# Performance work log

Hardware: AMD Instinct MI355X
Metric: run time of the kernel (lower is better)

The kernel has to match this reference:

```python
import jax, jax.numpy as jnp
import numpy as np

B, N, QD, H, D = 2, 2048, 1152, 16, 72
INNER = H * D
RETAIN_RATE = 0.4  # layer_count in [4, 64] branch
N_KEEP = int(N * RETAIN_RATE)
N_PRUNE = N - N_KEEP
SCALE = D ** (-0.5)


def setup_inputs() -> dict:
    key = jax.random.key(0)
    ks = jax.random.split(key, 6)
    s = 0.02
    return {
        "x": jax.random.normal(ks[0], (B, N, QD), jnp.float32),
        "Wq": jax.random.normal(ks[1], (QD, INNER), jnp.float32) * s,
        "Wk": jax.random.normal(ks[2], (QD, INNER), jnp.float32) * s,
        "Wv": jax.random.normal(ks[3], (QD, INNER), jnp.float32) * s,
        "Wo": jax.random.normal(ks[4], (INNER, QD), jnp.float32) * s,
        "bo": jnp.zeros((QD,), jnp.float32),
    }


def reference(x, Wq, Wk, Wv, Wo, bo):
    b = x.shape[0]
    # self-attention: context = x
    q = (x @ Wq).reshape(b, N, H, D).transpose(0, 2, 1, 3)  # [b,H,N,D]
    k = (x @ Wk).reshape(b, N, H, D).transpose(0, 2, 1, 3)
    v = (x @ Wv).reshape(b, N, H, D).transpose(0, 2, 1, 3)

    # ---- WPR pruning pass: full attention map, mean over heads ----
    logits = jnp.einsum('bhnd,bhmd->bhnm', q, k) * SCALE  # [b,H,N,N]
    M = jax.nn.softmax(logits, axis=-1)
    attn = M.mean(axis=1)  # [b,N,N]

    # 5-step power iteration: dist = (1/N) @ attn^5
    dist = jnp.full((b, 1, N), 1.0 / N, dtype=attn.dtype)
    for _ in range(5):
        dist = dist @ attn
    importance = dist[:, 0]  # [b,N]

    _, imp_inds = jax.lax.top_k(importance, N_KEEP)
    _, prune_inds = jax.lax.top_k(-importance, N_PRUNE)
    # boolean-mask selection in torch returns rows in ascending index order
    sorted_imp = jnp.sort(imp_inds, axis=1)      # [b,N_KEEP]
    sorted_prune = jnp.sort(prune_inds, axis=1)  # [b,N_PRUNE]

    selected_rows = jnp.take_along_axis(attn, sorted_imp[:, :, None], axis=1)  # [b,N_KEEP,N]
    max_inds = jnp.argmax(selected_rows, axis=1)  # [b,N]: most-attending retained row per token
    sim_inds = jnp.take_along_axis(max_inds, sorted_prune, axis=1)  # [b,N_PRUNE]

    # ---- attention among retained tokens only ----
    gi = sorted_imp[:, None, :, None]  # broadcast gather index
    q_r = jnp.take_along_axis(q, gi, axis=2)  # [b,H,N_KEEP,D]
    k_r = jnp.take_along_axis(k, gi, axis=2)
    v_r = jnp.take_along_axis(v, gi, axis=2)
    attn_r = jax.nn.softmax(jnp.einsum('bhnd,bhmd->bhnm', q_r, k_r) * SCALE, axis=-1)
    out_r = jnp.einsum('bhnm,bhmd->bhnd', attn_r, v_r)  # [b,H,N_KEEP,D]
    out_r = out_r.transpose(0, 2, 1, 3).reshape(b, N_KEEP, INNER)

    # similarity-based recovery for pruned tokens
    out_p = jnp.take_along_axis(out_r, sim_inds[:, :, None], axis=1)  # [b,N_PRUNE,INNER]

    bidx = jnp.arange(b)[:, None]
    out = jnp.zeros((b, N, INNER), out_r.dtype)
    out = out.at[bidx, sorted_imp].set(out_r)
    out = out.at[bidx, sorted_prune].set(out_p)

    return out @ Wo + bo
```

## Files before the change

### kernel.cpp

```cpp
#include <hip/hip_runtime.h>

namespace {
constexpr int B = 2;
constexpr int N = 2048;
constexpr int QD = 1152;
constexpr int H = 16;
constexpr int D = 72;
constexpr int INNER = 1152;
constexpr int NKEEP = 819;
constexpr int PSL = 32;
constexpr int ILEN = N / PSL;
constexpr int DP = 80;
constexpr int LSTR = 88;
constexpr int ASL = 8;
constexpr int ACH = (NKEEP + ASL - 1) / ASL;
}

#define FINF __builtin_inff()
#define SCALE 0.11785113019775793f

typedef __attribute__((ext_vector_type(8))) __bf16 bf16x8;
typedef __attribute__((ext_vector_type(16))) float f32x16;
typedef __attribute__((ext_vector_type(8))) short short8;

__device__ __forceinline__ f32x16 mfma_bf16(bf16x8 a, bf16x8 b, f32x16 c) {
  return __builtin_amdgcn_mfma_f32_32x32x16_bf16(a, b, c, 0, 0, 0);
}
__device__ __forceinline__ short f2bf(float x) {
  unsigned u = __float_as_uint(x);
  unsigned r = (u + 0x7fffu + ((u >> 16) & 1u)) >> 16;
  return (short)r;
}
__device__ __forceinline__ float bf2f(short b) {
  return __uint_as_float(((unsigned)(unsigned short)b) << 16);
}

__global__ __launch_bounds__(256) void k_xsplit(
    const float* __restrict__ X, short* __restrict__ Xh, short* __restrict__ Xl,
    int total)
{
  int g = blockIdx.x * 256 + threadIdx.x;
  if (g >= total) return;
  float v = X[g];
  short hb = f2bf(v);
  Xh[g] = hb;
  Xl[g] = f2bf(v - bf2f(hb));
}

__global__ __launch_bounds__(256) void k_wsplitT(
    const float* __restrict__ W, short* __restrict__ WTh, short* __restrict__ WTl)
{
  __shared__ float tile[64][65];
  const int tid = threadIdx.x;
  const int k0 = blockIdx.y * 64, n0 = blockIdx.x * 64;
  {
    int r = tid >> 2, c0 = (tid & 3) * 16;
#pragma unroll
    for (int j = 0; j < 16; j += 4) {
      float4 v = *(const float4*)&W[(size_t)(k0 + r) * 1152 + n0 + c0 + j];
      tile[r][c0 + j] = v.x; tile[r][c0 + j + 1] = v.y;
      tile[r][c0 + j + 2] = v.z; tile[r][c0 + j + 3] = v.w;
    }
  }
  __syncthreads();
  for (int e = tid; e < 4096; e += 256) {
    int nr = e >> 6, kc = e & 63;
    float v = tile[kc][nr];
    short hb = f2bf(v);
    WTh[(size_t)(n0 + nr) * 1152 + k0 + kc] = hb;
    WTl[(size_t)(n0 + nr) * 1152 + k0 + kc] = f2bf(v - bf2f(hb));
  }
}

__global__ __launch_bounds__(256, 2) void k_pgemm3(
    const short* __restrict__ Ah_g, const short* __restrict__ Al_g,
    const short* __restrict__ Bh_g, const short* __restrict__ Bl_g,
    short* __restrict__ QKV0)
{
  constexpr int LK = 40;
  __shared__ short AhS[256 * LK], AlS[256 * LK];
  __shared__ short BhS[128 * LK], BlS[128 * LK];
  const int tid = threadIdx.x;
  const int wv = tid >> 6, ln = tid & 63;
  const int col = ln & 31, hi = ln >> 5;
  const int wm = wv >> 1, wn = wv & 1;
  const int m0 = blockIdx.y * 256, n0 = blockIdx.x * 128;
  f32x16 acc[4][2];
#pragma unroll
  for (int mi = 0; mi < 4; ++mi)
#pragma unroll
    for (int ni = 0; ni < 2; ++ni)
#pragma unroll
      for (int r = 0; r < 16; ++r) acc[mi][ni][r] = 0.f;

  for (int kt = 0; kt < 1152; kt += 32) {
    __syncthreads();
    for (int e = tid; e < 1024; e += 256) {
      int r = e >> 2, c4 = e & 3;
      size_t sa = (size_t)(m0 + r) * 1152 + kt + c4 * 8;
      *(float4*)&AhS[r * LK + c4 * 8] = *(const float4*)(Ah_g + sa);
      *(float4*)&AlS[r * LK + c4 * 8] = *(const float4*)(Al_g + sa);
    }
    for (int e = tid; e < 512; e += 256) {
      int r = e >> 2, c4 = e & 3;
      size_t sb = (size_t)(n0 + r) * 1152 + kt + c4 * 8;
      *(float4*)&BhS[r * LK + c4 * 8] = *(const float4*)(Bh_g + sb);
      *(float4*)&BlS[r * LK + c4 * 8] = *(const float4*)(Bl_g + sb);
    }
    __syncthreads();
#pragma unroll
    for (int kc = 0; kc < 2; ++kc) {
      bf16x8 ah[4], al[4], bh[2], bl[2];
#pragma unroll
      for (int mi = 0; mi < 4; ++mi) {
        int r = wm * 128 + mi * 32 + col;
        ah[mi] = *(const bf16x8*)&AhS[r * LK + kc * 16 + hi * 8];
        al[mi] = *(const bf16x8*)&AlS[r * LK + kc * 16 + hi * 8];
      }
#pragma unroll
      for (int ni = 0; ni < 2; ++ni) {
        int r = wn * 64 + ni * 32 + col;
        bh[ni] = *(const bf16x8*)&BhS[r * LK + kc * 16 + hi * 8];
        bl[ni] = *(const bf16x8*)&BlS[r * LK + kc * 16 + hi * 8];
      }
#pragma unroll
      for (int mi = 0; mi < 4; ++mi)
#pragma unroll
        for (int ni = 0; ni < 2; ++ni) {
          acc[mi][ni] = mfma_bf16(ah[mi], bh[ni], acc[mi][ni]);
          acc[mi][ni] = mfma_bf16(ah[mi], bl[ni], acc[mi][ni]);
          acc[mi][ni] = mfma_bf16(al[mi], bh[ni], acc[mi][ni]);
        }
    }
  }
  const size_t S = (size_t)65536 * 80;
#pragma unroll
  for (int mi = 0; mi < 4; ++mi)
#pragma unroll
    for (int ni = 0; ni < 2; ++ni)
#pragma unroll
      for (int r = 0; r < 16; ++r) {
        int m = m0 + wm * 128 + mi * 32 + (r & 3) + 8 * (r >> 2) + 4 * hi;
        int c = n0 + wn * 64 + ni * 32 + col;
        int which = c / 1152, cm = c - which * 1152;
        int hh = cm / 72, dd = cm - hh * 72;
        int b = m >> 11, nn = m & 2047;
        size_t idx = (((size_t)(b * 16 + hh)) * 2048 + nn) * 80 + dd;
        float v = acc[mi][ni][r];
        short hb = f2bf(v);
        short* OH = QKV0 + (size_t)which * 2 * S;
        OH[idx] = hb;
        OH[S + idx] = f2bf(v - bf2f(hb));
      }
}

__global__ __launch_bounds__(256, 2) void k_stats3(
    const short* __restrict__ Qh, const short* __restrict__ Ql,
    const short* __restrict__ Kh, const short* __restrict__ Kl,
    float* __restrict__ inv_out)
{
  __shared__ __align__(16) short kh[64 * LSTR];
  __shared__ __align__(16) short kl[64 * LSTR];
  const int tid = threadIdx.x;
  const int wv = tid >> 6, ln = tid & 63;
  const int col = ln & 31, hi = ln >> 5;
  const int q0 = blockIdx.x * 256;
  const int h = blockIdx.y, b = blockIdx.z;
  const size_t bhbase = (size_t)(b * H + h) * N * DP;

  bf16x8 qfh[2][5], qfl[2][5];
#pragma unroll
  for (int mi = 0; mi < 2; ++mi) {
    const size_t rb = bhbase + (size_t)(q0 + wv * 64 + mi * 32 + col) * DP + hi * 8;
#pragma unroll
    for (int d = 0; d < 5; ++d) {
      qfh[mi][d] = *(const bf16x8*)(const void*)(Qh + rb + d * 16);
      qfl[mi][d] = *(const bf16x8*)(const void*)(Ql + rb + d * 16);
    }
  }
  float s[2][16];
#pragma unroll
  for (int mi = 0; mi < 2; ++mi)
#pragma unroll
    for (int r = 0; r < 16; ++r) s[mi][r] = 0.f;

  float4 rkh[3], rkl[3];
  auto LOADK = [&](int kt) {
#pragma unroll
    for (int ss = 0; ss < 3; ++ss) {
      int e = ss * 256 + tid;
      if (e < 640) {
        int r = e / 10, cc = e - r * 10;
        size_t sb = bhbase + (size_t)(kt + r) * DP + cc * 8;
        rkh[ss] = *(const float4*)(const void*)(Kh + sb);
        rkl[ss] = *(const float4*)(const void*)(Kl + sb);
      }
    }
  };
  auto STOREK = [&]() {
#pragma unroll
    for (int ss = 0; ss < 3; ++ss) {
      int e = ss * 256 + tid;
      if (e < 640) {
        int r = e / 10, cc = e - r * 10;
        *(float4*)(void*)(kh + r * LSTR + cc * 8) = rkh[ss];
        *(float4*)(void*)(kl + r * LSTR + cc * 8) = rkl[ss];
      }
    }
  };

  LOADK(0);
  for (int kt = 0; kt < N; kt += 64) {
    __syncthreads();
    STOREK();
    __syncthreads();
    if (kt + 64 < N) LOADK(kt + 64);
    f32x16 z[2][2];
#pragma unroll
    for (int mi = 0; mi < 2; ++mi)
#pragma unroll
      for (int rn = 0; rn < 2; ++rn)
#pragma unroll
        for (int r = 0; r < 16; ++r) z[mi][rn][r] = 0.f;
#pragma unroll
    for (int d = 0; d < 5; ++d) {
      const int boff = d * 16 + hi * 8;
      bf16x8 bh0 = *(const bf16x8*)(const void*)(kh + col * LSTR + boff);
      bf16x8 bl0 = *(const bf16x8*)(const void*)(kl + col * LSTR + boff);
      bf16x8 bh1 = *(const bf16x8*)(const void*)(kh + (32 + col) * LSTR + boff);
      bf16x8 bl1 = *(const bf16x8*)(const void*)(kl + (32 + col) * LSTR + boff);
#pragma unroll
      for (int mi = 0; mi < 2; ++mi) {
        z[mi][0] = mfma_bf16(qfh[mi][d], bh0, z[mi][0]);
        z[mi][0] = mfma_bf16(qfh[mi][d], bl0, z[mi][0]);
        z[mi][0] = mfma_bf16(qfl[mi][d], bh0, z[mi][0]);
        z[mi][1] = mfma_bf16(qfh[mi][d], bh1, z[mi][1]);
        z[mi][1] = mfma_bf16(qfh[mi][d], bl1, z[mi][1]);
        z[mi][1] = mfma_bf16(qfl[mi][d], bh1, z[mi][1]);
      }
    }
#pragma unroll
    for (int mi = 0; mi < 2; ++mi)
#pragma unroll
      for (int r = 0; r < 16; ++r)
        s[mi][r] += __expf(z[mi][0][r] * SCALE) + __expf(z[mi][1][r] * SCALE);
  }
#pragma unroll
  for (int mi = 0; mi < 2; ++mi)
#pragma unroll
    for (int r = 0; r < 16; ++r) {
      float v = s[mi][r];
#pragma unroll
      for (int o = 1; o < 32; o <<= 1) v += __shfl_xor(v, o);
      if (col == 0) {
        int row = q0 + wv * 64 + mi * 32 + ((r & 3) + ((r >> 2) << 3) + (hi << 2));
        inv_out[(size_t)(b * H + h) * N + row] = 1.0f / v;
      }
    }
}

__global__ __launch_bounds__(256, 2) void k_attn3(
    const short* __restrict__ Qh, const short* __restrict__ Ql,
    const short* __restrict__ Kh, const short* __restrict__ Kl,
    const float* __restrict__ inv_in, float* __restrict__ attn)
{
  __shared__ __align__(16) short kh[64 * LSTR];
  __shared__ __align__(16) short kl[64 * LSTR];
  __shared__ float invs[256];
  const int tid = threadIdx.x;
  const int wv = tid >> 6, ln = tid & 63;
  const int col = ln & 31, hi = ln >> 5;
  const int k0 = blockIdx.x * 64, q0 = blockIdx.y * 256, b = blockIdx.z;

  f32x16 pa[2][2];
#pragma unroll
  for (int mi = 0; mi < 2; ++mi)
#pragma unroll
    for (int rn = 0; rn < 2; ++rn)
#pragma unroll
      for (int r = 0; r < 16; ++r) pa[mi][rn][r] = 0.f;

  float4 rkh[3], rkl[3];
  float rin;
  auto LOADH = [&](int h) {
    const size_t hb = (size_t)(b * H + h) * N * DP;
#pragma unroll
    for (int ss = 0; ss < 3; ++ss) {
      int e = ss * 256 + tid;
      if (e < 640) {
        int r = e / 10, cc = e - r * 10;
        size_t sb = hb + (size_t)(k0 + r) * DP + cc * 8;
        rkh[ss] = *(const float4*)(const void*)(Kh + sb);
        rkl[ss] = *(const float4*)(const void*)(Kl + sb);
      }
    }
    rin = inv_in[(size_t)(b * H + h) * N + q0 + tid];
  };
  auto STOREH = [&]() {
#pragma unroll
    for (int ss = 0; ss < 3; ++ss) {
      int e = ss * 256 + tid;
      if (e < 640) {
        int r = e / 10, cc = e - r * 10;
        *(float4*)(void*)(kh + r * LSTR + cc * 8) = rkh[ss];
        *(float4*)(void*)(kl + r * LSTR + cc * 8) = rkl[ss];
      }
    }
    invs[tid] = rin;
  };

  LOADH(0);
  for (int h = 0; h < H; ++h) {
    __syncthreads();
    STOREH();
    __syncthreads();
    if (h + 1 < H) LOADH(h + 1);

    const size_t bhbase = (size_t)(b * H + h) * N * DP;
    f32x16 z[2][2];
#pragma unroll
    for (int mi = 0; mi < 2; ++mi)
#pragma unroll
      for (int rn = 0; rn < 2; ++rn)
#pragma unroll
        for (int r = 0; r < 16; ++r) z[mi][rn][r] = 0.f;

#pragma unroll
    for (int d = 0; d < 5; ++d) {
      const int boff = d * 16 + hi * 8;
      bf16x8 bh0 = *(const bf16x8*)(const void*)(kh + col * LSTR + boff);
      bf16x8 bl0 = *(const bf16x8*)(const void*)(kl + col * LSTR + boff);
      bf16x8 bh1 = *(const bf16x8*)(const void*)(kh + (32 + col) * LSTR + boff);
      bf16x8 bl1 = *(const bf16x8*)(const void*)(kl + (32 + col) * LSTR + boff);
      bf16x8 qh0 = *(const bf16x8*)(const void*)(Qh + bhbase + (size_t)(q0 + wv * 64 + col) * DP + boff);
      bf16x8 ql0 = *(const bf16x8*)(const void*)(Ql + bhbase + (size_t)(q0 + wv * 64 + col) * DP + boff);
      bf16x8 qh1 = *(const bf16x8*)(const void*)(Qh + bhbase + (size_t)(q0 + wv * 64 + 32 + col) * DP + boff);
      bf16x8 ql1 = *(const bf16x8*)(const void*)(Ql + bhbase + (size_t)(q0 + wv * 64 + 32 + col) * DP + boff);
      z[0][0] = mfma_bf16(qh0, bh0, z[0][0]);
      z[0][0] = mfma_bf16(qh0, bl0, z[0][0]);
      z[0][0] = mfma_bf16(ql0, bh0, z[0][0]);
      z[0][1] = mfma_bf16(qh0, bh1, z[0][1]);
      z[0][1] = mfma_bf16(qh0, bl1, z[0][1]);
      z[0][1] = mfma_bf16(ql0, bh1, z[0][1]);
      z[1][0] = mfma_bf16(qh1, bh0, z[1][0]);
      z[1][0] = mfma_bf16(qh1, bl0, z[1][0]);
      z[1][0] = mfma_bf16(ql1, bh0, z[1][0]);
      z[1][1] = mfma_bf16(qh1, bh1, z[1][1]);
      z[1][1] = mfma_bf16(qh1, bl1, z[1][1]);
      z[1][1] = mfma_bf16(ql1, bh1, z[1][1]);
    }
#pragma unroll
    for (int mi = 0; mi < 2; ++mi)
#pragma unroll
      for (int r = 0; r < 16; ++r) {
        const int rloc = wv * 64 + mi * 32 + (r & 3) + ((r >> 2) << 3) + (hi << 2);
        const float iv = invs[rloc];
        pa[mi][0][r] += __expf(z[mi][0][r] * SCALE) * iv;
        pa[mi][1][r] += __expf(z[mi][1][r] * SCALE) * iv;
      }
  }
  const float invH = 1.0f / H;
#pragma unroll
  for (int mi = 0; mi < 2; ++mi)
#pragma unroll
    for (int r = 0; r < 16; ++r) {
      const int row = q0 + wv * 64 + mi * 32 + (r & 3) + ((r >> 2) << 3) + (hi << 2);
      attn[((size_t)b * N + row) * N + k0 + col] = pa[mi][0][r] * invH;
      attn[((size_t)b * N + row) * N + k0 + 32 + col] = pa[mi][1][r] * invH;
    }
}

__global__ __launch_bounds__(256) void k_power(
    const float* __restrict__ attn, const float* __restrict__ din,
    float* __restrict__ partial, int first)
{
  int g = blockIdx.x * 256 + threadIdx.x;
  int sy = blockIdx.y;
  int b = g / N, j = g % N;
  const float* ab = attn + (size_t)b * N * N;
  int i0 = sy * ILEN;
  float sum = 0.f;
  if (first) {
    for (int i = i0; i < i0 + ILEN; ++i) sum += ab[(size_t)i * N + j];
    sum *= (1.0f / N);
  } else {
    const float* db = din + b * N;
    for (int i = i0; i < i0 + ILEN; ++i) sum += db[i] * ab[(size_t)i * N + j];
  }
  partial[(size_t)sy * (B * N) + g] = sum;
}

__global__ __launch_bounds__(256) void k_powred(
    const float* __restrict__ partial, float* __restrict__ dout)
{
  int g = blockIdx.x * 256 + threadIdx.x;
  if (g >= B * N) return;
  float s = 0.f;
  for (int sy = 0; sy < PSL; ++sy) s += partial[(size_t)sy * (B * N) + g];
  dout[g] = s;
}

__global__ __launch_bounds__(1024) void k_partition(
    const float* __restrict__ imp, int* __restrict__ sorted_imp,
    int* __restrict__ keepflag, int* __restrict__ s_map)
{
  __shared__ float v[N];
  __shared__ int   id[N];
  __shared__ int   kf[N];
  __shared__ int   ps[N];
  const int tid = threadIdx.x;
  const int b = blockIdx.x;
  for (int i = tid; i < N; i += 1024) { v[i] = imp[b * N + i]; id[i] = i; }
  for (int k = 2; k <= N; k <<= 1) {
    for (int j = k >> 1; j > 0; j >>= 1) {
      __syncthreads();
      for (int i = tid; i < N; i += 1024) {
        int ixj = i ^ j;
        if (ixj > i) {
          bool up = ((i & k) == 0);
          float va = v[i], vb = v[ixj];
          int ia = id[i], ib = id[ixj];
          bool b_before_a = (vb > va) || (vb == va && ib < ia);
          if (b_before_a == up) { v[i] = vb; v[ixj] = va; id[i] = ib; id[ixj] = ia; }
        }
      }
    }
  }
  __syncthreads();
  for (int i = tid; i < N; i += 1024) kf[id[i]] = (i < NKEEP) ? 1 : 0;
  __syncthreads();
  for (int i = tid; i < N; i += 1024) ps[i] = kf[i];
  for (int off = 1; off < N; off <<= 1) {
    __syncthreads();
    int t0 = (tid >= off) ? ps[tid - off] : 0;
    int i1 = tid + 1024;
    int t1 = ps[i1 - off];
    __syncthreads();
    ps[tid] += t0;
    ps[i1] += t1;
  }
  __syncthreads();
  for (int i = tid; i < N; i += 1024) {
    int excl = ps[i] - kf[i];
    keepflag[b * N + i] = kf[i];
    if (kf[i]) { sorted_imp[b * NKEEP + excl] = i; s_map[b * N + i] = excl; }
  }
}

__global__ __launch_bounds__(256) void k_argmax_part(
    const float* __restrict__ attn, const int* __restrict__ sorted_imp,
    float* __restrict__ pval, int* __restrict__ pidx)
{
  __shared__ int imp_s[ACH];
  const int tid = threadIdx.x;
  const int g = blockIdx.x * 256 + tid;
  const int s = blockIdx.y;
  const int b = g / N, n = g % N;
  const int k0 = s * ACH;
  const int k1 = (k0 + ACH < NKEEP) ? k0 + ACH : NKEEP;
  const int cnt = k1 - k0;
  for (int i = tid; i < cnt; i += 256) imp_s[i] = sorted_imp[b * NKEEP + k0 + i];
  __syncthreads();
  const float* ab = attn + (size_t)b * N * N;
  float best = -FINF; int bi = k0;
  for (int k = 0; k < cnt; ++k) {
    float val = ab[(size_t)imp_s[k] * N + n];
    if (val > best) { best = val; bi = k0 + k; }
  }
  pval[(size_t)s * (B * N) + g] = best;
  pidx[(size_t)s * (B * N) + g] = bi;
}

__global__ __launch_bounds__(256) void k_argmax_comb(
    const float* __restrict__ pval, const int* __restrict__ pidx,
    const int* __restrict__ keepflag, int* __restrict__ s_map)
{
  int g = blockIdx.x * 256 + threadIdx.x;
  if (g >= B * N) return;
  float best = -FINF; int bi = 0;
#pragma unroll
  for (int s = 0; s < ASL; ++s) {
    float v = pval[(size_t)s * (B * N) + g];
    if (v > best) { best = v; bi = pidx[(size_t)s * (B * N) + g]; }
  }
  if (!keepflag[g]) s_map[g] = bi;
}

__global__ __launch_bounds__(256, 2) void k_rfused(
    const short* __restrict__ Qh, const short* __restrict__ Ql,
    const short* __restrict__ Kh, const short* __restrict__ Kl,
    const short* __restrict__ Vh, const int* __restrict__ sorted_imp,
    short* __restrict__ Yh, short* __restrict__ Yl)
{
  constexpr int LK = 88;
  constexpr int VTS = 72;
  __shared__ __align__(16) short KhS[64 * LK];
  __shared__ __align__(16) short KlS[64 * LK];
  __shared__ __align__(16) short VhS[64 * LK];
  __shared__ __align__(16) short VT[72 * VTS];
  __shared__ int imp[NKEEP];
  const int tid = threadIdx.x;
  const int wv = tid >> 6, ln = tid & 63;
  const int col = ln & 31, hi = ln >> 5;
  const int b = blockIdx.z, h = blockIdx.y, q0 = blockIdx.x * 128;
  const size_t bh80 = (size_t)(b * H + h) * N * DP;
  for (int i = tid; i < NKEEP; i += 256) imp[i] = sorted_imp[b * NKEEP + i];
  __syncthreads();
  int qr = q0 + wv * 32 + col;
  int qi = imp[qr < NKEEP ? qr : NKEEP - 1];
  bf16x8 qfh[5], qfl[5];
  {
    const size_t qb = bh80 + (size_t)qi * DP + hi * 8;
#pragma unroll
    for (int d = 0; d < 5; ++d) {
      qfh[d] = *(const bf16x8*)(const void*)(Qh + qb + d * 16);
      qfl[d] = *(const bf16x8*)(const void*)(Ql + qb + d * 16);
    }
  }
  float denom = 0.f;
  f32x16 oacc[3];
#pragma unroll
  for (int nc = 0; nc < 3; ++nc)
#pragma unroll
    for (int r = 0; r < 16; ++r) oacc[nc][r] = 0.f;

  for (int kt = 0; kt < 832; kt += 64) {
    for (int e = tid; e < 640; e += 256) {
      int r = e / 10, cc = e - r * 10;
      int kv = kt + r;
      float4 vkh, vkl, vvh;
      if (kv < NKEEP) {
        size_t sb = bh80 + (size_t)imp[kv] * DP + cc * 8;
        vkh = *(const float4*)(const void*)(Kh + sb);
        vkl = *(const float4*)(const void*)(Kl + sb);
        vvh = *(const float4*)(const void*)(Vh + sb);
      } else {
        vkh = make_float4(0.f, 0.f, 0.f, 0.f); vkl = vkh; vvh = vkh;
      }
      *(float4*)(void*)&KhS[r * LK + cc * 8] = vkh;
      *(float4*)(void*)&KlS[r * LK + cc * 8] = vkl;
      *(float4*)(void*)&VhS[r * LK + cc * 8] = vvh;
    }
    __syncthreads();
    f32x16 z[2];
#pragma unroll
    for (int rn = 0; rn < 2; ++rn)
#pragma unroll
      for (int r = 0; r < 16; ++r) z[rn][r] = 0.f;
#pragma unroll
    for (int d = 0; d < 5; ++d) {
      const int boff = d * 16 + hi * 8;
#pragma unroll
      for (int rn = 0; rn < 2; ++rn) {
        bf16x8 kfh = *(const bf16x8*)(const void*)(KhS + (rn * 32 + col) * LK + boff);
        bf16x8 kfl = *(const bf16x8*)(const void*)(KlS + (rn * 32 + col) * LK + boff);
        z[rn] = mfma_bf16(kfh, qfh[d], z[rn]);
        z[rn] = mfma_bf16(kfh, qfl[d], z[rn]);
        z[rn] = mfma_bf16(kfl, qfh[d], z[rn]);
      }
    }
    for (int e = tid; e < 576; e += 256) {
      int dd = e % 72, k8 = e / 72;
      short8 t;
#pragma unroll
      for (int j = 0; j < 8; ++j) t[j] = VhS[(k8 * 8 + j) * LK + dd];
      *(short8*)(void*)&VT[dd * VTS + k8 * 8] = t;
    }
    const bool full = (kt + 64 <= NKEEP);
#pragma unroll
    for (int rn = 0; rn < 2; ++rn) {
      int kvb = kt + rn * 32 + 4 * hi;
#pragma unroll
      for (int r = 0; r < 16; ++r) {
        float pe = __expf(z[rn][r] * SCALE);
        if (!full) {
          int kv = kvb + (r & 3) + 8 * (r >> 2);
          pe = (kv < NKEEP) ? pe : 0.f;
        }
        z[rn][r] = pe;
        denom += pe;
      }
    }
    __syncthreads();
#pragma unroll
    for (int rn = 0; rn < 2; ++rn) {
#pragma unroll
      for (int kc = 0; kc < 2; ++kc) {
        unsigned p0, p1, p2, p3;
        asm("v_cvt_pk_bf16_f32 %0, %1, %2" : "=v"(p0) : "v"(z[rn][8 * kc + 0]), "v"(z[rn][8 * kc + 1]));
        asm("v_cvt_pk_bf16_f32 %0, %1, %2" : "=v"(p1) : "v"(z[rn][8 * kc + 2]), "v"(z[rn][8 * kc + 3]));
        asm("v_cvt_pk_bf16_f32 %0, %1, %2" : "=v"(p2) : "v"(z[rn][8 * kc + 4]), "v"(z[rn][8 * kc + 5]));
        asm("v_cvt_pk_bf16_f32 %0, %1, %2" : "=v"(p3) : "v"(z[rn][8 * kc + 6]), "v"(z[rn][8 * kc + 7]));
        unsigned othA = hi ? p0 : p2, othB = hi ? p1 : p3;
        unsigned swA = (unsigned)__shfl_xor((int)othA, 32);
        unsigned swB = (unsigned)__shfl_xor((int)othB, 32);
        union { unsigned u[4]; bf16x8 v; } pf;
        pf.u[0] = hi ? swA : p0; pf.u[1] = hi ? swB : p1;
        pf.u[2] = hi ? p2 : swA; pf.u[3] = hi ? p3 : swB;
        const int kb = rn * 32 + kc * 16 + hi * 8;
#pragma unroll
        for (int nc = 0; nc < 3; ++nc) {
          int dr = nc * 32 + col; if (dr > 71) dr = 71;
          bf16x8 vf = *(const bf16x8*)(const void*)(VT + dr * VTS + kb);
          oacc[nc] = mfma_bf16(pf.v, vf, oacc[nc]);
        }
      }
    }
  }
  denom += __shfl_xor(denom, 32);
  float invd = 1.0f / denom;
#pragma unroll
  for (int r = 0; r < 16; ++r) {
    int cr = (r & 3) + 8 * (r >> 2) + 4 * hi;
    int q = q0 + wv * 32 + cr;
    float dv = __shfl(invd, cr);
    if (q < NKEEP) {
#pragma unroll
      for (int nc = 0; nc < 3; ++nc) {
        int dd = nc * 32 + col;
        if (dd < 72) {
          float v = oacc[nc][r] * dv;
          size_t idx = ((size_t)b * NKEEP + q) * 1152 + h * 72 + dd;
          short hb = f2bf(v);
          Yh[idx] = hb;
          Yl[idx] = f2bf(v - bf2f(hb));
        }
      }
    }
  }
}

__global__ __launch_bounds__(256, 2) void k_pgemm(
    const short* __restrict__ Ah_g, const short* __restrict__ Al_g,
    const short* __restrict__ Bh_g, const short* __restrict__ Bl_g,
    float* __restrict__ OutF, const float* __restrict__ bias,
    int Mtot)
{
  constexpr int LK = 40;
  __shared__ short AhS[128 * LK], AlS[128 * LK], BhS[128 * LK], BlS[128 * LK];
  const int tid = threadIdx.x;
  const int wv = tid >> 6, ln = tid & 63;
  const int col = ln & 31, hi = ln >> 5;
  const int wm = wv >> 1, wn = wv & 1;
  const int m0 = blockIdx.y * 128, n0 = blockIdx.x * 128;
  f32x16 acc[2][2];
#pragma unroll
  for (int mi = 0; mi < 2; ++mi)
#pragma unroll
    for (int ni = 0; ni < 2; ++ni)
#pragma unroll
      for (int r = 0; r < 16; ++r) acc[mi][ni][r] = 0.f;

  for (int kt = 0; kt < 1152; kt += 32) {
    __syncthreads();
    for (int e = tid; e < 512; e += 256) {
      int r = e >> 2, c4 = e & 3;
      int ra = m0 + r; if (ra >= Mtot) ra = Mtot - 1;
      size_t sa = (size_t)ra * 1152 + kt + c4 * 8;
      *(float4*)&AhS[r * LK + c4 * 8] = *(const float4*)(Ah_g + sa);
      *(float4*)&AlS[r * LK + c4 * 8] = *(const float4*)(Al_g + sa);
      size_t sb = (size_t)(n0 + r) * 1152 + kt + c4 * 8;
      *(float4*)&BhS[r * LK + c4 * 8] = *(const float4*)(Bh_g + sb);
      *(float4*)&BlS[r * LK + c4 * 8] = *(const float4*)(Bl_g + sb);
    }
    __syncthreads();
#pragma unroll
    for (int kc = 0; kc < 2; ++kc) {
      bf16x8 ah[2], al[2], bh[2], bl[2];
#pragma unroll
      for (int mi = 0; mi < 2; ++mi) {
        int r = wm * 64 + mi * 32 + col;
        ah[mi] = *(const bf16x8*)&AhS[r * LK + kc * 16 + hi * 8];
        al[mi] = *(const bf16x8*)&AlS[r * LK + kc * 16 + hi * 8];
      }
#pragma unroll
      for (int ni = 0; ni < 2; ++ni) {
        int r = wn * 64 + ni * 32 + col;
        bh[ni] = *(const bf16x8*)&BhS[r * LK + kc * 16 + hi * 8];
        bl[ni] = *(const bf16x8*)&BlS[r * LK + kc * 16 + hi * 8];
      }
#pragma unroll
      for (int mi = 0; mi < 2; ++mi)
#pragma unroll
        for (int ni = 0; ni < 2; ++ni) {
          acc[mi][ni] = mfma_bf16(ah[mi], bh[ni], acc[mi][ni]);
          acc[mi][ni] = mfma_bf16(ah[mi], bl[ni], acc[mi][ni]);
          acc[mi][ni] = mfma_bf16(al[mi], bh[ni], acc[mi][ni]);
        }
    }
  }
#pragma unroll
  for (int mi = 0; mi < 2; ++mi)
#pragma unroll
    for (int ni = 0; ni < 2; ++ni)
#pragma unroll
      for (int r = 0; r < 16; ++r) {
        int m = m0 + wm * 64 + mi * 32 + (r & 3) + 8 * (r >> 2) + 4 * hi;
        int c = n0 + wn * 64 + ni * 32 + col;
        if (m < Mtot) OutF[(size_t)m * 1152 + c] = acc[mi][ni][r] + bias[c];
      }
}

__global__ __launch_bounds__(256) void k_scatter(
    const float* __restrict__ Y, const int* __restrict__ s_map,
    float* __restrict__ out)
{
  size_t g = (size_t)blockIdx.x * 256 + threadIdx.x;
  if (g >= (size_t)B * N * QD) return;
  int c = (int)(g % QD);
  int n_ = (int)((g / QD) % N);
  int b = (int)(g / ((size_t)N * QD));
  int src = s_map[b * N + n_];
  out[g] = Y[((size_t)b * NKEEP + src) * QD + c];
}

extern "C" void kernel_launch(void* const* d_in, const int* in_sizes, int n_in,
                              void* d_out, int out_size, void* d_ws, size_t ws_size,
                              hipStream_t stream)
{
  const float* x  = (const float*)d_in[0];
  const float* Wq = (const float*)d_in[1];
  const float* Wk = (const float*)d_in[2];
  const float* Wv = (const float*)d_in[3];
  const float* Wo = (const float*)d_in[4];
  const float* bo = (const float*)d_in[5];
  float* out = (float*)d_out;

  char* ws = (char*)d_ws;
  size_t off = 0;
  auto alloc = [&](size_t bytes) -> void* {
    void* p = ws + off;
    off = (off + bytes + 255) & ~(size_t)255;
    return p;
  };
  const int ROWS = B * H * N;
  const size_t XEL = (size_t)B * N * QD;
  const size_t WEL = (size_t)QD * INNER;
  short* xh   = (short*)alloc(sizeof(short) * XEL);
  short* xl   = (short*)alloc(sizeof(short) * XEL);
  short* WTh  = (short*)alloc(sizeof(short) * WEL * 3);
  short* WTl  = (short*)alloc(sizeof(short) * WEL * 3);
  short* Qhb  = (short*)alloc(sizeof(short) * (size_t)ROWS * DP);
  short* Qlb  = (short*)alloc(sizeof(short) * (size_t)ROWS * DP);
  short* Khb  = (short*)alloc(sizeof(short) * (size_t)ROWS * DP);
  short* Klb  = (short*)alloc(sizeof(short) * (size_t)ROWS * DP);
  short* Vhb  = (short*)alloc(sizeof(short) * (size_t)ROWS * DP);
  short* Vlb  = (short*)alloc(sizeof(short) * (size_t)ROWS * DP);
  float* attn = (float*)alloc(sizeof(float) * (size_t)B * N * N);
  float* inv  = (float*)alloc(sizeof(float) * (size_t)ROWS);
  float* d0   = (float*)alloc(sizeof(float) * B * N);
  float* d1   = (float*)alloc(sizeof(float) * B * N);
  float* partial = (float*)alloc(sizeof(float) * PSL * B * N);
  int* sorted_imp = (int*)alloc(sizeof(int) * B * NKEEP);
  int* keepflag   = (int*)alloc(sizeof(int) * B * N);
  int* s_map      = (int*)alloc(sizeof(int) * B * N);
  float* pval     = (float*)alloc(sizeof(float) * ASL * B * N);
  int*   pidx     = (int*)alloc(sizeof(int) * ASL * B * N);
  (void)Vlb;
  short* Yh = xh;
  short* Yl = xh + (size_t)B * NKEEP * INNER;
  float* Y  = (float*)xl;

  dim3 blk(256);

  k_xsplit<<<dim3(((int)XEL + 255) / 256), blk, 0, stream>>>(x, xh, xl, (int)XEL);
  dim3 wg(QD / 64, QD / 64);
  k_wsplitT<<<wg, blk, 0, stream>>>(Wq, WTh, WTl);
  k_wsplitT<<<wg, blk, 0, stream>>>(Wk, WTh + WEL, WTl + WEL);
  k_wsplitT<<<wg, blk, 0, stream>>>(Wv, WTh + 2 * WEL, WTl + 2 * WEL);

  hipMemsetAsync(Qhb, 0, sizeof(short) * (size_t)ROWS * DP * 6, stream);

  k_pgemm3<<<dim3(3 * INNER / 128, (B * N) / 256), blk, 0, stream>>>(
      xh, xl, WTh, WTl, Qhb);

  k_wsplitT<<<wg, blk, 0, stream>>>(Wo, WTh, WTl);

  k_stats3<<<dim3(N / 256, H, B), blk, 0, stream>>>(Qhb, Qlb, Khb, Klb, inv);
  k_attn3<<<dim3(N / 64, N / 256, B), blk, 0, stream>>>(Qhb, Qlb, Khb, Klb, inv, attn);

  k_power<<<dim3(B * N / 256, PSL), blk, 0, stream>>>(attn, nullptr, partial, 1);
  k_powred<<<dim3(B * N / 256), blk, 0, stream>>>(partial, d0);
  float* src = d0; float* dst = d1;
  for (int it = 1; it < 5; ++it) {
    k_power<<<dim3(B * N / 256, PSL), blk, 0, stream>>>(attn, src, partial, 0);
    k_powred<<<dim3(B * N / 256), blk, 0, stream>>>(partial, dst);
    float* t = src; src = dst; dst = t;
  }

  k_partition<<<dim3(B), dim3(1024), 0, stream>>>(src, sorted_imp, keepflag, s_map);
  k_argmax_part<<<dim3(B * N / 256, ASL), blk, 0, stream>>>(attn, sorted_imp, pval, pidx);
  k_argmax_comb<<<dim3(B * N / 256), blk, 0, stream>>>(pval, pidx, keepflag, s_map);

  k_rfused<<<dim3((NKEEP + 127) / 128, H, B), blk, 0, stream>>>(
      Qhb, Qlb, Khb, Klb, Vhb, sorted_imp, Yh, Yl);

  k_pgemm<<<dim3(QD / 128, (B * NKEEP + 127) / 128), blk, 0, stream>>>(
      Yh, Yl, WTh, WTl, Y, bo, B * NKEEP);
  k_scatter<<<dim3((int)(((size_t)B * N * QD + 255) / 256)), blk, 0, stream>>>(Y, s_map, out);
}
```

Before: 585.1 us.

## Fuse power-iteration reductions, batch weight splits, and shrink GEMM tiles

Folds the partial-sum reduction of each power-iteration step into the next step's matvec kernel, cutting four reduce launches. The three Q/K/V weight split-transposes become one 3D-grid launch. The QKV GEMM tile drops from 256x128 to 128x128 and the output GEMM from 128x128 to 64x64, giving more blocks for better CU occupancy. The cost is redundant partial reads in every block and lower per-block data reuse in the GEMMs.

```diff
diff --git a/kernel.cpp b/kernel.cpp
--- a/kernel.cpp
+++ b/kernel.cpp
@@ -47,6 +47,35 @@
   Xl[g] = f2bf(v - bf2f(hb));
 }
 
+__global__ __launch_bounds__(256) void k_wsplit3(
+    const float* __restrict__ W0, const float* __restrict__ W1,
+    const float* __restrict__ W2, short* __restrict__ WTh, short* __restrict__ WTl)
+{
+  __shared__ float tile[64][65];
+  const int tid = threadIdx.x;
+  const int k0 = blockIdx.y * 64, n0 = blockIdx.x * 64;
+  const int z = blockIdx.z;
+  const float* W = (z == 0) ? W0 : (z == 1) ? W1 : W2;
+  const size_t zoff = (size_t)z * QD * INNER;
+  {
+    int r = tid >> 2, c0 = (tid & 3) * 16;
+#pragma unroll
+    for (int j = 0; j < 16; j += 4) {
+      float4 v = *(const float4*)&W[(size_t)(k0 + r) * 1152 + n0 + c0 + j];
+      tile[r][c0 + j] = v.x; tile[r][c0 + j + 1] = v.y;
+      tile[r][c0 + j + 2] = v.z; tile[r][c0 + j + 3] = v.w;
+    }
+  }
+  __syncthreads();
+  for (int e = tid; e < 4096; e += 256) {
+    int nr = e >> 6, kc = e & 63;
+    float v = tile[kc][nr];
+    short hb = f2bf(v);
+    WTh[zoff + (size_t)(n0 + nr) * 1152 + k0 + kc] = hb;
+    WTl[zoff + (size_t)(n0 + nr) * 1152 + k0 + kc] = f2bf(v - bf2f(hb));
+  }
+}
+
 __global__ __launch_bounds__(256) void k_wsplitT(
     const float* __restrict__ W, short* __restrict__ WTh, short* __restrict__ WTl)
 {
@@ -78,16 +107,15 @@
     short* __restrict__ QKV0)
 {
   constexpr int LK = 40;
-  __shared__ short AhS[256 * LK], AlS[256 * LK];
-  __shared__ short BhS[128 * LK], BlS[128 * LK];
+  __shared__ short AhS[128 * LK], AlS[128 * LK], BhS[128 * LK], BlS[128 * LK];
   const int tid = threadIdx.x;
   const int wv = tid >> 6, ln = tid & 63;
   const int col = ln & 31, hi = ln >> 5;
   const int wm = wv >> 1, wn = wv & 1;
-  const int m0 = blockIdx.y * 256, n0 = blockIdx.x * 128;
-  f32x16 acc[4][2];
-#pragma unroll
-  for (int mi = 0; mi < 4; ++mi)
+  const int m0 = blockIdx.y * 128, n0 = blockIdx.x * 128;
+  f32x16 acc[2][2];
+#pragma unroll
+  for (int mi = 0; mi < 2; ++mi)
 #pragma unroll
     for (int ni = 0; ni < 2; ++ni)
 #pragma unroll
@@ -95,14 +123,11 @@
 
   for (int kt = 0; kt < 1152; kt += 32) {
     __syncthreads();
-    for (int e = tid; e < 1024; e += 256) {
+    for (int e = tid; e < 512; e += 256) {
       int r = e >> 2, c4 = e & 3;
       size_t sa = (size_t)(m0 + r) * 1152 + kt + c4 * 8;
       *(float4*)&AhS[r * LK + c4 * 8] = *(const float4*)(Ah_g + sa);
       *(float4*)&AlS[r * LK + c4 * 8] = *(const float4*)(Al_g + sa);
-    }
-    for (int e = tid; e < 512; e += 256) {
-      int r = e >> 2, c4 = e & 3;
       size_t sb = (size_t)(n0 + r) * 1152 + kt + c4 * 8;
       *(float4*)&BhS[r * LK + c4 * 8] = *(const float4*)(Bh_g + sb);
       *(float4*)&BlS[r * LK + c4 * 8] = *(const float4*)(Bl_g + sb);
@@ -110,10 +135,10 @@
     __syncthreads();
 #pragma unroll
     for (int kc = 0; kc < 2; ++kc) {
-      bf16x8 ah[4], al[4], bh[2], bl[2];
-#pragma unroll
-      for (int mi = 0; mi < 4; ++mi) {
-        int r = wm * 128 + mi * 32 + col;
+      bf16x8 ah[2], al[2], bh[2], bl[2];
+#pragma unroll
+      for (int mi = 0; mi < 2; ++mi) {
+        int r = wm * 64 + mi * 32 + col;
         ah[mi] = *(const bf16x8*)&AhS[r * LK + kc * 16 + hi * 8];
         al[mi] = *(const bf16x8*)&AlS[r * LK + kc * 16 + hi * 8];
       }
@@ -124,7 +149,7 @@
         bl[ni] = *(const bf16x8*)&BlS[r * LK + kc * 16 + hi * 8];
       }
 #pragma unroll
-      for (int mi = 0; mi < 4; ++mi)
+      for (int mi = 0; mi < 2; ++mi)
 #pragma unroll
         for (int ni = 0; ni < 2; ++ni) {
           acc[mi][ni] = mfma_bf16(ah[mi], bh[ni], acc[mi][ni]);
@@ -135,12 +160,12 @@
   }
   const size_t S = (size_t)65536 * 80;
 #pragma unroll
-  for (int mi = 0; mi < 4; ++mi)
+  for (int mi = 0; mi < 2; ++mi)
 #pragma unroll
     for (int ni = 0; ni < 2; ++ni)
 #pragma unroll
       for (int r = 0; r < 16; ++r) {
-        int m = m0 + wm * 128 + mi * 32 + (r & 3) + 8 * (r >> 2) + 4 * hi;
+        int m = m0 + wm * 64 + mi * 32 + (r & 3) + 8 * (r >> 2) + 4 * hi;
         int c = n0 + wn * 64 + ni * 32 + col;
         int which = c / 1152, cm = c - which * 1152;
         int hh = cm / 72, dd = cm - hh * 72;
@@ -371,8 +396,7 @@
 }
 
 __global__ __launch_bounds__(256) void k_power(
-    const float* __restrict__ attn, const float* __restrict__ din,
-    float* __restrict__ partial, int first)
+    const float* __restrict__ attn, float* __restrict__ partial)
 {
   int g = blockIdx.x * 256 + threadIdx.x;
   int sy = blockIdx.y;
@@ -380,14 +404,36 @@
   const float* ab = attn + (size_t)b * N * N;
   int i0 = sy * ILEN;
   float sum = 0.f;
-  if (first) {
-    for (int i = i0; i < i0 + ILEN; ++i) sum += ab[(size_t)i * N + j];
-    sum *= (1.0f / N);
-  } else {
-    const float* db = din + b * N;
-    for (int i = i0; i < i0 + ILEN; ++i) sum += db[i] * ab[(size_t)i * N + j];
-  }
-  partial[(size_t)sy * (B * N) + g] = sum;
+  for (int i = i0; i < i0 + ILEN; ++i) sum += ab[(size_t)i * N + j];
+  partial[(size_t)sy * (B * N) + g] = sum * (1.0f / N);
+}
+
+__global__ __launch_bounds__(256) void k_powfused(
+    const float* __restrict__ attn, const float* __restrict__ partial_in,
+    float* __restrict__ partial_out)
+{
+  __shared__ float red[4][64];
+  __shared__ float ds[64];
+  const int tid = threadIdx.x;
+  const int g = blockIdx.x * 256 + tid;
+  const int sy = blockIdx.y;
+  const int b = g / N, j = g % N;
+  const int i0 = sy * ILEN;
+  {
+    int i = tid & 63, sgrp = tid >> 6;
+    const float* p = partial_in + (size_t)(b * N + i0 + i);
+    float s8 = 0.f;
+#pragma unroll
+    for (int k = 0; k < 8; ++k) s8 += p[(size_t)(sgrp * 8 + k) * (B * N)];
+    red[sgrp][i] = s8;
+  }
+  __syncthreads();
+  if (tid < 64) ds[tid] = red[0][tid] + red[1][tid] + red[2][tid] + red[3][tid];
+  __syncthreads();
+  const float* ab = attn + (size_t)b * N * N;
+  float sum = 0.f;
+  for (int i = 0; i < ILEN; ++i) sum += ds[i] * ab[(size_t)(i0 + i) * N + j];
+  partial_out[(size_t)sy * (B * N) + g] = sum;
 }
 
 __global__ __launch_bounds__(256) void k_powred(
@@ -630,30 +676,27 @@
   }
 }
 
-__global__ __launch_bounds__(256, 2) void k_pgemm(
+__global__ __launch_bounds__(256, 2) void k_ogemm(
     const short* __restrict__ Ah_g, const short* __restrict__ Al_g,
     const short* __restrict__ Bh_g, const short* __restrict__ Bl_g,
     float* __restrict__ OutF, const float* __restrict__ bias,
     int Mtot)
 {
   constexpr int LK = 40;
-  __shared__ short AhS[128 * LK], AlS[128 * LK], BhS[128 * LK], BlS[128 * LK];
+  __shared__ short AhS[64 * LK], AlS[64 * LK], BhS[64 * LK], BlS[64 * LK];
   const int tid = threadIdx.x;
   const int wv = tid >> 6, ln = tid & 63;
   const int col = ln & 31, hi = ln >> 5;
   const int wm = wv >> 1, wn = wv & 1;
-  const int m0 = blockIdx.y * 128, n0 = blockIdx.x * 128;
-  f32x16 acc[2][2];
-#pragma unroll
-  for (int mi = 0; mi < 2; ++mi)
-#pragma unroll
-    for (int ni = 0; ni < 2; ++ni)
-#pragma unroll
-      for (int r = 0; r < 16; ++r) acc[mi][ni][r] = 0.f;
+  const int m0 = blockIdx.y * 64, n0 = blockIdx.x * 64;
+  f32x16 acc;
+#pragma unroll
+  for (int r = 0; r < 16; ++r) acc[r] = 0.f;
 
   for (int kt = 0; kt < 1152; kt += 32) {
     __syncthreads();
-    for (int e = tid; e < 512; e += 256) {
+    {
+      int e = tid;
       int r = e >> 2, c4 = e & 3;
       int ra = m0 + r; if (ra >= Mtot) ra = Mtot - 1;
       size_t sa = (size_t)ra * 1152 + kt + c4 * 8;
@@ -666,39 +709,23 @@
     __syncthreads();
 #pragma unroll
     for (int kc = 0; kc < 2; ++kc) {
-      bf16x8 ah[2], al[2], bh[2], bl[2];
-#pragma unroll
-      for (int mi = 0; mi < 2; ++mi) {
-        int r = wm * 64 + mi * 32 + col;
-        ah[mi] = *(const bf16x8*)&AhS[r * LK + kc * 16 + hi * 8];
-        al[mi] = *(const bf16x8*)&AlS[r * LK + kc * 16 + hi * 8];
-      }
-#pragma unroll
-      for (int ni = 0; ni < 2; ++ni) {
-        int r = wn * 64 + ni * 32 + col;
-        bh[ni] = *(const bf16x8*)&BhS[r * LK + kc * 16 + hi * 8];
-        bl[ni] = *(const bf16x8*)&BlS[r * LK + kc * 16 + hi * 8];
-      }
-#pragma unroll
-      for (int mi = 0; mi < 2; ++mi)
-#pragma unroll
-        for (int ni = 0; ni < 2; ++ni) {
-          acc[mi][ni] = mfma_bf16(ah[mi], bh[ni], acc[mi][ni]);
-          acc[mi][ni] = mfma_bf16(ah[mi], bl[ni], acc[mi][ni]);
-          acc[mi][ni] = mfma_bf16(al[mi], bh[ni], acc[mi][ni]);
-        }
-    }
-  }
-#pragma unroll
-  for (int mi = 0; mi < 2; ++mi)
-#pragma unroll
-    for (int ni = 0; ni < 2; ++ni)
-#pragma unroll
-      for (int r = 0; r < 16; ++r) {
-        int m = m0 + wm * 64 + mi * 32 + (r & 3) + 8 * (r >> 2) + 4 * hi;
-        int c = n0 + wn * 64 + ni * 32 + col;
-        if (m < Mtot) OutF[(size_t)m * 1152 + c] = acc[mi][ni][r] + bias[c];
-      }
+      int ra = wm * 32 + col;
+      int rb = wn * 32 + col;
+      bf16x8 ah = *(const bf16x8*)&AhS[ra * LK + kc * 16 + hi * 8];
+      bf16x8 al = *(const bf16x8*)&AlS[ra * LK + kc * 16 + hi * 8];
+      bf16x8 bh = *(const bf16x8*)&BhS[rb * LK + kc * 16 + hi * 8];
+      bf16x8 bl = *(const bf16x8*)&BlS[rb * LK + kc * 16 + hi * 8];
+      acc = mfma_bf16(ah, bh, acc);
+      acc = mfma_bf16(ah, bl, acc);
+      acc = mfma_bf16(al, bh, acc);
+    }
+  }
+#pragma unroll
+  for (int r = 0; r < 16; ++r) {
+    int m = m0 + wm * 32 + (r & 3) + 8 * (r >> 2) + 4 * hi;
+    int c = n0 + wn * 32 + col;
+    if (m < Mtot) OutF[(size_t)m * 1152 + c] = acc[r] + bias[c];
+  }
 }
 
 __global__ __launch_bounds__(256) void k_scatter(
@@ -748,9 +775,9 @@
   short* Vlb  = (short*)alloc(sizeof(short) * (size_t)ROWS * DP);
   float* attn = (float*)alloc(sizeof(float) * (size_t)B * N * N);
   float* inv  = (float*)alloc(sizeof(float) * (size_t)ROWS);
-  float* d0   = (float*)alloc(sizeof(float) * B * N);
-  float* d1   = (float*)alloc(sizeof(float) * B * N);
-  float* partial = (float*)alloc(sizeof(float) * PSL * B * N);
+  float* dvec = (float*)alloc(sizeof(float) * B * N);
+  float* partA = (float*)alloc(sizeof(float) * PSL * B * N);
+  float* partB = (float*)alloc(sizeof(float) * PSL * B * N);
   int* sorted_imp = (int*)alloc(sizeof(int) * B * NKEEP);
   int* keepflag   = (int*)alloc(sizeof(int) * B * N);
   int* s_map      = (int*)alloc(sizeof(int) * B * N);
@@ -764,38 +791,33 @@
   dim3 blk(256);
 
   k_xsplit<<<dim3(((int)XEL + 255) / 256), blk, 0, stream>>>(x, xh, xl, (int)XEL);
-  dim3 wg(QD / 64, QD / 64);
-  k_wsplitT<<<wg, blk, 0, stream>>>(Wq, WTh, WTl);
-  k_wsplitT<<<wg, blk, 0, stream>>>(Wk, WTh + WEL, WTl + WEL);
-  k_wsplitT<<<wg, blk, 0, stream>>>(Wv, WTh + 2 * WEL, WTl + 2 * WEL);
+  k_wsplit3<<<dim3(QD / 64, QD / 64, 3), blk, 0, stream>>>(Wq, Wk, Wv, WTh, WTl);
 
   hipMemsetAsync(Qhb, 0, sizeof(short) * (size_t)ROWS * DP * 6, stream);
 
-  k_pgemm3<<<dim3(3 * INNER / 128, (B * N) / 256), blk, 0, stream>>>(
+  k_pgemm3<<<dim3(3 * INNER / 128, (B * N) / 128), blk, 0, stream>>>(
       xh, xl, WTh, WTl, Qhb);
 
-  k_wsplitT<<<wg, blk, 0, stream>>>(Wo, WTh, WTl);
+  k_wsplitT<<<dim3(QD / 64, QD / 64), blk, 0, stream>>>(Wo, WTh, WTl);
 
   k_stats3<<<dim3(N / 256, H, B), blk, 0, stream>>>(Qhb, Qlb, Khb, Klb, inv);
   k_attn3<<<dim3(N / 64, N / 256, B), blk, 0, stream>>>(Qhb, Qlb, Khb, Klb, inv, attn);
 
-  k_power<<<dim3(B * N / 256, PSL), blk, 0, stream>>>(attn, nullptr, partial, 1);
-  k_powred<<<dim3(B * N / 256), blk, 0, stream>>>(partial, d0);
-  float* src = d0; float* dst = d1;
-  for (int it = 1; it < 5; ++it) {
-    k_power<<<dim3(B * N / 256, PSL), blk, 0, stream>>>(attn, src, partial, 0);
-    k_powred<<<dim3(B * N / 256), blk, 0, stream>>>(partial, dst);
-    float* t = src; src = dst; dst = t;
-  }
-
-  k_partition<<<dim3(B), dim3(1024), 0, stream>>>(src, sorted_imp, keepflag, s_map);
+  k_power<<<dim3(B * N / 256, PSL), blk, 0, stream>>>(attn, partA);
+  k_powfused<<<dim3(B * N / 256, PSL), blk, 0, stream>>>(attn, partA, partB);
+  k_powfused<<<dim3(B * N / 256, PSL), blk, 0, stream>>>(attn, partB, partA);
+  k_powfused<<<dim3(B * N / 256, PSL), blk, 0, stream>>>(attn, partA, partB);
+  k_powfused<<<dim3(B * N / 256, PSL), blk, 0, stream>>>(attn, partB, partA);
+  k_powred<<<dim3(B * N / 256), blk, 0, stream>>>(partA, dvec);
+
+  k_partition<<<dim3(B), dim3(1024), 0, stream>>>(dvec, sorted_imp, keepflag, s_map);
   k_argmax_part<<<dim3(B * N / 256, ASL), blk, 0, stream>>>(attn, sorted_imp, pval, pidx);
   k_argmax_comb<<<dim3(B * N / 256), blk, 0, stream>>>(pval, pidx, keepflag, s_map);
 
   k_rfused<<<dim3((NKEEP + 127) / 128, H, B), blk, 0, stream>>>(
       Qhb, Qlb, Khb, Klb, Vhb, sorted_imp, Yh, Yl);
 
-  k_pgemm<<<dim3(QD / 128, (B * NKEEP + 127) / 128), blk, 0, stream>>>(
+  k_ogemm<<<dim3(QD / 64, (B * NKEEP + 63) / 64), blk, 0, stream>>>(
       Yh, Yl, WTh, WTl, Y, bo, B * NKEEP);
   k_scatter<<<dim3((int)(((size_t)B * N * QD + 255) / 256)), blk, 0, stream>>>(Y, s_map, out);
 }
```

After: 562.3 us. -3.9%, faster.
